# Optimization experiments

Hardware: AMD Instinct MI355X
Metric: run time of the kernel (lower is better)

Reference implementation:

```python
import jax, jax.numpy as jnp
import numpy as np

N_EMBED = 1024
HEAD_SIZE = 64

def setup_inputs() -> dict:
    key = jax.random.key(0)
    kx, kq, kk, kv = jax.random.split(key, 4)
    B, T = 8, 2048
    s = 1.0 / np.sqrt(N_EMBED)
    return {
        "x": jax.random.normal(kx, (B, T, N_EMBED), dtype=jnp.float32),
        "Wq": jax.random.normal(kq, (N_EMBED, HEAD_SIZE), dtype=jnp.float32) * s,
        "Wk": jax.random.normal(kk, (N_EMBED, HEAD_SIZE), dtype=jnp.float32) * s,
        "Wv": jax.random.normal(kv, (N_EMBED, HEAD_SIZE), dtype=jnp.float32) * s,
    }

def reference(x, Wq, Wk, Wv):
    # x: [B,T,C]; W*: [C,H]
    q = x @ Wq  # [B,T,H]
    k = x @ Wk
    v = x @ Wv
    T = x.shape[1]
    scale = jnp.asarray(HEAD_SIZE, x.dtype) ** -0.5
    wei = jnp.einsum("bth,bsh->bts", q, k) * scale  # [B,T,T]
    causal = jnp.tril(jnp.ones((T, T), dtype=bool))
    wei = jnp.where(causal, wei, jnp.asarray(-jnp.inf, wei.dtype))
    wei = jax.nn.softmax(wei, axis=-1)
    # dropout = 0.0 (eval mode): identity
    return jnp.einsum("bts,bsh->bth", wei, v)  # [B,T,H]
```

## Files before the change

kernel.cpp:

```cpp
#include <hip/hip_runtime.h>

#define NB 8
#define NT 2048
#define NC 1024
#define NH 64

typedef __bf16 bf16x8 __attribute__((ext_vector_type(8)));
typedef float f32x4 __attribute__((ext_vector_type(4)));

static __device__ __forceinline__ float4 ldf4(const float* p) {
  return *reinterpret_cast<const float4*>(p);
}
static __device__ __forceinline__ unsigned pack_bf2(float a, float b) {
  unsigned short ua = __builtin_bit_cast(unsigned short, (__bf16)a);
  unsigned short ub = __builtin_bit_cast(unsigned short, (__bf16)b);
  return (unsigned)ua | ((unsigned)ub << 16);
}

__global__ __launch_bounds__(256) void wt_kernel(
    const float* __restrict__ Wq, const float* __restrict__ Wk,
    const float* __restrict__ Wv, __bf16* __restrict__ wt) {
  __shared__ __bf16 tl[64][72];
  const int tid = threadIdx.x;
  const int mat = blockIdx.x >> 4;
  const int k0 = (blockIdx.x & 15) * 64;
  const float* W = (mat == 0) ? Wq : (mat == 1) ? Wk : Wv;
#pragma unroll
  for (int it = 0; it < 4; ++it) {
    int f = tid + it * 256;
    int kk = f >> 4, c4 = (f & 15) * 4;
    float4 w = ldf4(&W[(k0 + kk) * NH + c4]);
    tl[c4 + 0][kk] = (__bf16)w.x;
    tl[c4 + 1][kk] = (__bf16)w.y;
    tl[c4 + 2][kk] = (__bf16)w.z;
    tl[c4 + 3][kk] = (__bf16)w.w;
  }
  __syncthreads();
#pragma unroll
  for (int it = 0; it < 2; ++it) {
    int f = tid + it * 256;
    int h = f >> 3, k8 = (f & 7) * 8;
    *reinterpret_cast<bf16x8*>(&wt[(mat * 64 + h) * NC + k0 + k8]) =
        *reinterpret_cast<const bf16x8*>(&tl[h][k8]);
  }
}

__global__ __launch_bounds__(256, 2) void qkv_mfma_kernel(
    const float* __restrict__ x, const __bf16* __restrict__ wt,
    __bf16* __restrict__ qb, __bf16* __restrict__ kb, __bf16* __restrict__ vt) {
  __shared__ __bf16 As[32][72];
  __shared__ __bf16 Bs[192][72];
  __shared__ __bf16 vls[64][40];
  const int tid = threadIdx.x;
  const int lane = tid & 63;
  const int w = tid >> 6;
  const int row0 = blockIdx.x * 32;
  const int csub = w * 48;
  const int l15 = lane & 15, lg = lane >> 4;

  f32x4 acc[2][3];
#pragma unroll
  for (int i = 0; i < 2; ++i)
#pragma unroll
    for (int j = 0; j < 3; ++j) acc[i][j] = (f32x4){0.f, 0.f, 0.f, 0.f};

  float4 areg[2];
  bf16x8 breg[6];
#pragma unroll
  for (int it = 0; it < 2; ++it) {
    int f = tid + it * 256;
    int r = f >> 4, k4 = (f & 15) * 4;
    areg[it] = ldf4(&x[(row0 + r) * NC + k4]);
  }
#pragma unroll
  for (int it = 0; it < 6; ++it) {
    int f = tid + it * 256;
    int col = f >> 3, k8 = (f & 7) * 8;
    breg[it] = *reinterpret_cast<const bf16x8*>(&wt[col * NC + k8]);
  }

  for (int ch = 0; ch < 16; ++ch) {
#pragma unroll
    for (int it = 0; it < 2; ++it) {
      int f = tid + it * 256;
      int r = f >> 4, k4 = (f & 15) * 4;
      uint2 u = {pack_bf2(areg[it].x, areg[it].y), pack_bf2(areg[it].z, areg[it].w)};
      *reinterpret_cast<uint2*>(&As[r][k4]) = u;
    }
#pragma unroll
    for (int it = 0; it < 6; ++it) {
      int f = tid + it * 256;
      int col = f >> 3, k8 = (f & 7) * 8;
      *reinterpret_cast<bf16x8*>(&Bs[col][k8]) = breg[it];
    }
    __syncthreads();
    if (ch < 15) {
      const int k0n = (ch + 1) * 64;
#pragma unroll
      for (int it = 0; it < 2; ++it) {
        int f = tid + it * 256;
        int r = f >> 4, k4 = (f & 15) * 4;
        areg[it] = ldf4(&x[(row0 + r) * NC + k0n + k4]);
      }
#pragma unroll
      for (int it = 0; it < 6; ++it) {
        int f = tid + it * 256;
        int col = f >> 3, k8 = (f & 7) * 8;
        breg[it] = *reinterpret_cast<const bf16x8*>(&wt[col * NC + k0n + k8]);
      }
    }
#pragma unroll
    for (int kk = 0; kk < 2; ++kk) {
      bf16x8 af[2], bfr[3];
#pragma unroll
      for (int rt = 0; rt < 2; ++rt)
        af[rt] = *reinterpret_cast<const bf16x8*>(&As[rt * 16 + l15][kk * 32 + lg * 8]);
#pragma unroll
      for (int nt = 0; nt < 3; ++nt)
        bfr[nt] = *reinterpret_cast<const bf16x8*>(&Bs[csub + nt * 16 + l15][kk * 32 + lg * 8]);
#pragma unroll
      for (int rt = 0; rt < 2; ++rt)
#pragma unroll
        for (int nt = 0; nt < 3; ++nt)
          acc[rt][nt] = __builtin_amdgcn_mfma_f32_16x16x32_bf16(af[rt], bfr[nt], acc[rt][nt], 0, 0, 0);
    }
    __syncthreads();
  }

#pragma unroll
  for (int rt = 0; rt < 2; ++rt) {
#pragma unroll
    for (int nt = 0; nt < 3; ++nt) {
      int colbase = csub + nt * 16;
      int mat = colbase >> 6;
      int h = (colbase & 63) + l15;
      if (mat == 0) {
#pragma unroll
        for (int r = 0; r < 4; ++r) {
          int row = row0 + rt * 16 + lg * 4 + r;
          qb[row * NH + h] = (__bf16)(acc[rt][nt][r] * 0.125f);
        }
      } else if (mat == 1) {
#pragma unroll
        for (int r = 0; r < 4; ++r) {
          int row = row0 + rt * 16 + lg * 4 + r;
          kb[row * NH + h] = (__bf16)acc[rt][nt][r];
        }
      } else {
        ushort4 pk;
        pk.x = __builtin_bit_cast(unsigned short, (__bf16)acc[rt][nt][0]);
        pk.y = __builtin_bit_cast(unsigned short, (__bf16)acc[rt][nt][1]);
        pk.z = __builtin_bit_cast(unsigned short, (__bf16)acc[rt][nt][2]);
        pk.w = __builtin_bit_cast(unsigned short, (__bf16)acc[rt][nt][3]);
        *reinterpret_cast<ushort4*>(&vls[h][rt * 16 + lg * 4]) = pk;
      }
    }
  }
  __syncthreads();
  {
    int h = tid >> 2, t8 = (tid & 3) * 8;
    int bb = row0 >> 11;
    int t0l = row0 & (NT - 1);
    *reinterpret_cast<bf16x8*>(&vt[((size_t)bb * NH + h) * NT + t0l + t8]) =
        *reinterpret_cast<const bf16x8*>(&vls[h][t8]);
  }
}

__global__ __launch_bounds__(256, 2) void attn_mfma_kernel(
    const __bf16* __restrict__ qb, const __bf16* __restrict__ kb,
    const __bf16* __restrict__ vt, float* __restrict__ out) {
  __shared__ __bf16 ps[4][32][72];
  __shared__ float obuf[4][32][68];
  __shared__ float msh[4][32], lsh[4][32];
  const int tid = threadIdx.x;
  const int lane = tid & 63;
  const int w = tid >> 6;
  const int l15 = lane & 15, lg = lane >> 4;
  const int b = blockIdx.y;
  const int qt = (blockIdx.y < 4) ? (63 - (int)blockIdx.x) : (int)blockIdx.x;
  const int q0 = qt * 32;
  const size_t bT = (size_t)b * NT;

  bf16x8 qf[2][2];
#pragma unroll
  for (int ct = 0; ct < 2; ++ct)
#pragma unroll
    for (int kh = 0; kh < 2; ++kh)
      qf[ct][kh] = *reinterpret_cast<const bf16x8*>(
          &qb[(bT + q0 + ct * 16 + l15) * NH + kh * 32 + lg * 8]);

  float m[2] = {-1e30f, -1e30f};
  float lsum[2] = {0.f, 0.f};
  f32x4 o[2][4];
#pragma unroll
  for (int i = 0; i < 2; ++i)
#pragma unroll
    for (int j = 0; j < 4; ++j) o[i][j] = (f32x4){0.f, 0.f, 0.f, 0.f};

  const int nch = qt / 2 + 1;
  bf16x8 kf[4][2], vf[4][2];
  if (w < nch) {
    const int s0 = w * 64;
#pragma unroll
    for (int st = 0; st < 4; ++st)
#pragma unroll
      for (int kh = 0; kh < 2; ++kh)
        kf[st][kh] = *reinterpret_cast<const bf16x8*>(
            &kb[(bT + s0 + st * 16 + l15) * NH + kh * 32 + lg * 8]);
#pragma unroll
    for (int ht = 0; ht < 4; ++ht)
#pragma unroll
      for (int sh = 0; sh < 2; ++sh)
        vf[ht][sh] = *reinterpret_cast<const bf16x8*>(
            &vt[((size_t)b * NH + ht * 16 + l15) * NT + s0 + sh * 32 + lg * 8]);
  }

  for (int c = w; c < nch; c += 4) {
    const int s0 = c * 64;
    f32x4 s[4][2];
#pragma unroll
    for (int st = 0; st < 4; ++st)
#pragma unroll
      for (int ct = 0; ct < 2; ++ct) s[st][ct] = (f32x4){0.f, 0.f, 0.f, 0.f};
    __builtin_amdgcn_s_setprio(1);
#pragma unroll
    for (int st = 0; st < 4; ++st)
#pragma unroll
      for (int ct = 0; ct < 2; ++ct)
#pragma unroll
        for (int kh = 0; kh < 2; ++kh)
          s[st][ct] = __builtin_amdgcn_mfma_f32_16x16x32_bf16(kf[st][kh], qf[ct][kh], s[st][ct], 0, 0, 0);
    __builtin_amdgcn_s_setprio(0);

    const int cn = c + 4;
    bf16x8 kfn[4][2], vfn[4][2];
    if (cn < nch) {
      const int sn = cn * 64;
#pragma unroll
      for (int st = 0; st < 4; ++st)
#pragma unroll
        for (int kh = 0; kh < 2; ++kh)
          kfn[st][kh] = *reinterpret_cast<const bf16x8*>(
              &kb[(bT + sn + st * 16 + l15) * NH + kh * 32 + lg * 8]);
#pragma unroll
      for (int ht = 0; ht < 4; ++ht)
#pragma unroll
        for (int sh = 0; sh < 2; ++sh)
          vfn[ht][sh] = *reinterpret_cast<const bf16x8*>(
              &vt[((size_t)b * NH + ht * 16 + l15) * NT + sn + sh * 32 + lg * 8]);
    }

    if (s0 + 63 > q0) {
#pragma unroll
      for (int st = 0; st < 4; ++st)
#pragma unroll
        for (int ct = 0; ct < 2; ++ct) {
          int qg = q0 + ct * 16 + l15;
#pragma unroll
          for (int r = 0; r < 4; ++r) {
            int sg = s0 + st * 16 + lg * 4 + r;
            if (sg > qg) s[st][ct][r] = -1e30f;
          }
        }
    }
    float scv[2];
#pragma unroll
    for (int ct = 0; ct < 2; ++ct) {
      float rmx = -1e30f;
#pragma unroll
      for (int st = 0; st < 4; ++st)
#pragma unroll
        for (int r = 0; r < 4; ++r) rmx = fmaxf(rmx, s[st][ct][r]);
      rmx = fmaxf(rmx, __shfl_xor(rmx, 16));
      rmx = fmaxf(rmx, __shfl_xor(rmx, 32));
      float mn = fmaxf(m[ct], rmx);
      float sc = __expf(m[ct] - mn);
      m[ct] = mn;
      float rs = 0.f;
#pragma unroll
      for (int st = 0; st < 4; ++st) {
        float p0 = __expf(s[st][ct][0] - mn);
        float p1 = __expf(s[st][ct][1] - mn);
        float p2 = __expf(s[st][ct][2] - mn);
        float p3 = __expf(s[st][ct][3] - mn);
        rs += (p0 + p1) + (p2 + p3);
        int sp = st * 16 + lg * 4;
        *reinterpret_cast<unsigned*>(&ps[w][ct * 16 + l15][sp]) = pack_bf2(p0, p1);
        *reinterpret_cast<unsigned*>(&ps[w][ct * 16 + l15][sp + 2]) = pack_bf2(p2, p3);
      }
      rs += __shfl_xor(rs, 16);
      rs += __shfl_xor(rs, 32);
      lsum[ct] = lsum[ct] * sc + rs;
      scv[ct] = sc;
    }
#pragma unroll
    for (int rt = 0; rt < 2; ++rt)
#pragma unroll
      for (int r = 0; r < 4; ++r) {
        float fsc = __shfl(scv[rt], lg * 4 + r, 64);
#pragma unroll
        for (int ht = 0; ht < 4; ++ht) o[rt][ht][r] *= fsc;
      }
    __builtin_amdgcn_s_setprio(1);
#pragma unroll
    for (int rt = 0; rt < 2; ++rt) {
      bf16x8 pf[2];
#pragma unroll
      for (int sh = 0; sh < 2; ++sh)
        pf[sh] = *reinterpret_cast<const bf16x8*>(&ps[w][rt * 16 + l15][sh * 32 + lg * 8]);
#pragma unroll
      for (int ht = 0; ht < 4; ++ht)
#pragma unroll
        for (int sh = 0; sh < 2; ++sh)
          o[rt][ht] = __builtin_amdgcn_mfma_f32_16x16x32_bf16(pf[sh], vf[ht][sh], o[rt][ht], 0, 0, 0);
    }
    __builtin_amdgcn_s_setprio(0);
    if (cn < nch) {
#pragma unroll
      for (int st = 0; st < 4; ++st)
#pragma unroll
        for (int kh = 0; kh < 2; ++kh) kf[st][kh] = kfn[st][kh];
#pragma unroll
      for (int ht = 0; ht < 4; ++ht)
#pragma unroll
        for (int sh = 0; sh < 2; ++sh) vf[ht][sh] = vfn[ht][sh];
    }
  }

  if (lg == 0) {
#pragma unroll
    for (int ct = 0; ct < 2; ++ct) {
      msh[w][ct * 16 + l15] = m[ct];
      lsh[w][ct * 16 + l15] = lsum[ct];
    }
  }
#pragma unroll
  for (int rt = 0; rt < 2; ++rt)
#pragma unroll
    for (int ht = 0; ht < 4; ++ht)
#pragma unroll
      for (int r = 0; r < 4; ++r)
        obuf[w][rt * 16 + lg * 4 + r][ht * 16 + l15] = o[rt][ht][r];
  __syncthreads();

  {
    int qr = tid >> 3, h8 = (tid & 7) * 8;
    float m0 = msh[0][qr], m1 = msh[1][qr], m2 = msh[2][qr], m3 = msh[3][qr];
    float M = fmaxf(fmaxf(m0, m1), fmaxf(m2, m3));
    float e0 = __expf(m0 - M), e1 = __expf(m1 - M);
    float e2 = __expf(m2 - M), e3 = __expf(m3 - M);
    float L = e0 * lsh[0][qr] + e1 * lsh[1][qr] + e2 * lsh[2][qr] + e3 * lsh[3][qr];
    float inv = 1.f / L;
#pragma unroll
    for (int i = 0; i < 8; ++i) {
      int h = h8 + i;
      float v = e0 * obuf[0][qr][h] + e1 * obuf[1][qr][h] +
                e2 * obuf[2][qr][h] + e3 * obuf[3][qr][h];
      out[(bT + q0 + qr) * NH + h] = v * inv;
    }
  }
}

extern "C" void kernel_launch(void* const* d_in, const int* in_sizes, int n_in,
                              void* d_out, int out_size, void* d_ws, size_t ws_size,
                              hipStream_t stream) {
  const float* x  = (const float*)d_in[0];
  const float* Wq = (const float*)d_in[1];
  const float* Wk = (const float*)d_in[2];
  const float* Wv = (const float*)d_in[3];
  float* out = (float*)d_out;

  char* ws = (char*)d_ws;
  __bf16* wt = (__bf16*)(ws);
  __bf16* qb = (__bf16*)(ws + 393216);
  __bf16* kb = (__bf16*)(ws + 393216 + 2097152);
  __bf16* vt = (__bf16*)(ws + 393216 + 2 * 2097152);

  wt_kernel<<<dim3(48), dim3(256), 0, stream>>>(Wq, Wk, Wv, wt);
  qkv_mfma_kernel<<<dim3(512), dim3(256), 0, stream>>>(x, wt, qb, kb, vt);
  attn_mfma_kernel<<<dim3(64, 8), dim3(256), 0, stream>>>(qb, kb, vt, out);
}
```

Before: 48.06 us.

## Halve attention query tile to 16 rows, doubling blocks and occupancy

The attention kernel now processes 16 query rows per block instead of 32 and launches 128x8 blocks. Launch bounds rise from 2 to 4 blocks per SM, and the explicit K/V register prefetch for the next chunk is removed, which frees registers. The final output store is vectorised to float4. More blocks should improve load balance and latency hiding on the causal workload. The cost is that each K/V chunk is reloaded by twice as many blocks, and without the prefetch, load latency is exposed inside each iteration.

```diff
diff --git a/kernel.cpp b/kernel.cpp
--- a/kernel.cpp
+++ b/kernel.cpp
@@ -166,198 +166,144 @@
   }
 }
 
-__global__ __launch_bounds__(256, 2) void attn_mfma_kernel(
+__global__ __launch_bounds__(256, 4) void attn_mfma_kernel(
     const __bf16* __restrict__ qb, const __bf16* __restrict__ kb,
     const __bf16* __restrict__ vt, float* __restrict__ out) {
-  __shared__ __bf16 ps[4][32][72];
-  __shared__ float obuf[4][32][68];
-  __shared__ float msh[4][32], lsh[4][32];
+  __shared__ __bf16 ps[4][16][88];
+  __shared__ float obuf[4][16][68];
+  __shared__ float msh[4][16], lsh[4][16];
   const int tid = threadIdx.x;
   const int lane = tid & 63;
   const int w = tid >> 6;
   const int l15 = lane & 15, lg = lane >> 4;
   const int b = blockIdx.y;
-  const int qt = (blockIdx.y < 4) ? (63 - (int)blockIdx.x) : (int)blockIdx.x;
-  const int q0 = qt * 32;
+  const int qt = ((blockIdx.y & 3) < 2) ? (127 - (int)blockIdx.x) : (int)blockIdx.x;
+  const int q0 = qt * 16;
   const size_t bT = (size_t)b * NT;
 
-  bf16x8 qf[2][2];
-#pragma unroll
-  for (int ct = 0; ct < 2; ++ct)
-#pragma unroll
-    for (int kh = 0; kh < 2; ++kh)
-      qf[ct][kh] = *reinterpret_cast<const bf16x8*>(
-          &qb[(bT + q0 + ct * 16 + l15) * NH + kh * 32 + lg * 8]);
-
-  float m[2] = {-1e30f, -1e30f};
-  float lsum[2] = {0.f, 0.f};
-  f32x4 o[2][4];
-#pragma unroll
-  for (int i = 0; i < 2; ++i)
-#pragma unroll
-    for (int j = 0; j < 4; ++j) o[i][j] = (f32x4){0.f, 0.f, 0.f, 0.f};
-
-  const int nch = qt / 2 + 1;
-  bf16x8 kf[4][2], vf[4][2];
-  if (w < nch) {
-    const int s0 = w * 64;
+  bf16x8 qf[2];
+#pragma unroll
+  for (int kh = 0; kh < 2; ++kh)
+    qf[kh] = *reinterpret_cast<const bf16x8*>(
+        &qb[(bT + q0 + l15) * NH + kh * 32 + lg * 8]);
+
+  float m = -1e30f, lsum = 0.f;
+  f32x4 o[4];
+#pragma unroll
+  for (int j = 0; j < 4; ++j) o[j] = (f32x4){0.f, 0.f, 0.f, 0.f};
+
+  const int nch = qt / 4 + 1;
+  for (int c = w; c < nch; c += 4) {
+    const int s0 = c * 64;
+    bf16x8 kf[4][2];
 #pragma unroll
     for (int st = 0; st < 4; ++st)
 #pragma unroll
       for (int kh = 0; kh < 2; ++kh)
         kf[st][kh] = *reinterpret_cast<const bf16x8*>(
             &kb[(bT + s0 + st * 16 + l15) * NH + kh * 32 + lg * 8]);
+    f32x4 s[4];
+#pragma unroll
+    for (int st = 0; st < 4; ++st) s[st] = (f32x4){0.f, 0.f, 0.f, 0.f};
+    __builtin_amdgcn_s_setprio(1);
+#pragma unroll
+    for (int st = 0; st < 4; ++st)
+#pragma unroll
+      for (int kh = 0; kh < 2; ++kh)
+        s[st] = __builtin_amdgcn_mfma_f32_16x16x32_bf16(kf[st][kh], qf[kh], s[st], 0, 0, 0);
+    __builtin_amdgcn_s_setprio(0);
+
+    bf16x8 vf[4][2];
 #pragma unroll
     for (int ht = 0; ht < 4; ++ht)
 #pragma unroll
       for (int sh = 0; sh < 2; ++sh)
         vf[ht][sh] = *reinterpret_cast<const bf16x8*>(
             &vt[((size_t)b * NH + ht * 16 + l15) * NT + s0 + sh * 32 + lg * 8]);
-  }
-
-  for (int c = w; c < nch; c += 4) {
-    const int s0 = c * 64;
-    f32x4 s[4][2];
+
+    if (s0 + 63 > q0) {
+      const int qg = q0 + l15;
+#pragma unroll
+      for (int st = 0; st < 4; ++st)
+#pragma unroll
+        for (int r = 0; r < 4; ++r) {
+          int sg = s0 + st * 16 + lg * 4 + r;
+          if (sg > qg) s[st][r] = -1e30f;
+        }
+    }
+    float rmx = -1e30f;
 #pragma unroll
     for (int st = 0; st < 4; ++st)
 #pragma unroll
-      for (int ct = 0; ct < 2; ++ct) s[st][ct] = (f32x4){0.f, 0.f, 0.f, 0.f};
+      for (int r = 0; r < 4; ++r) rmx = fmaxf(rmx, s[st][r]);
+    rmx = fmaxf(rmx, __shfl_xor(rmx, 16));
+    rmx = fmaxf(rmx, __shfl_xor(rmx, 32));
+    float mn = fmaxf(m, rmx);
+    float sc = __expf(m - mn);
+    m = mn;
+    float rs = 0.f;
+#pragma unroll
+    for (int st = 0; st < 4; ++st) {
+      float p0 = __expf(s[st][0] - mn);
+      float p1 = __expf(s[st][1] - mn);
+      float p2 = __expf(s[st][2] - mn);
+      float p3 = __expf(s[st][3] - mn);
+      rs += (p0 + p1) + (p2 + p3);
+      int sp = st * 16 + lg * 4;
+      *reinterpret_cast<unsigned*>(&ps[w][l15][sp]) = pack_bf2(p0, p1);
+      *reinterpret_cast<unsigned*>(&ps[w][l15][sp + 2]) = pack_bf2(p2, p3);
+    }
+    rs += __shfl_xor(rs, 16);
+    rs += __shfl_xor(rs, 32);
+    lsum = lsum * sc + rs;
+#pragma unroll
+    for (int r = 0; r < 4; ++r) {
+      float fsc = __shfl(sc, lg * 4 + r, 64);
+#pragma unroll
+      for (int ht = 0; ht < 4; ++ht) o[ht][r] *= fsc;
+    }
     __builtin_amdgcn_s_setprio(1);
-#pragma unroll
-    for (int st = 0; st < 4; ++st)
-#pragma unroll
-      for (int ct = 0; ct < 2; ++ct)
-#pragma unroll
-        for (int kh = 0; kh < 2; ++kh)
-          s[st][ct] = __builtin_amdgcn_mfma_f32_16x16x32_bf16(kf[st][kh], qf[ct][kh], s[st][ct], 0, 0, 0);
+    bf16x8 pf[2];
+#pragma unroll
+    for (int sh = 0; sh < 2; ++sh)
+      pf[sh] = *reinterpret_cast<const bf16x8*>(&ps[w][l15][sh * 32 + lg * 8]);
+#pragma unroll
+    for (int ht = 0; ht < 4; ++ht)
+#pragma unroll
+      for (int sh = 0; sh < 2; ++sh)
+        o[ht] = __builtin_amdgcn_mfma_f32_16x16x32_bf16(pf[sh], vf[ht][sh], o[ht], 0, 0, 0);
     __builtin_amdgcn_s_setprio(0);
-
-    const int cn = c + 4;
-    bf16x8 kfn[4][2], vfn[4][2];
-    if (cn < nch) {
-      const int sn = cn * 64;
-#pragma unroll
-      for (int st = 0; st < 4; ++st)
-#pragma unroll
-        for (int kh = 0; kh < 2; ++kh)
-          kfn[st][kh] = *reinterpret_cast<const bf16x8*>(
-              &kb[(bT + sn + st * 16 + l15) * NH + kh * 32 + lg * 8]);
-#pragma unroll
-      for (int ht = 0; ht < 4; ++ht)
-#pragma unroll
-        for (int sh = 0; sh < 2; ++sh)
-          vfn[ht][sh] = *reinterpret_cast<const bf16x8*>(
-              &vt[((size_t)b * NH + ht * 16 + l15) * NT + sn + sh * 32 + lg * 8]);
-    }
-
-    if (s0 + 63 > q0) {
-#pragma unroll
-      for (int st = 0; st < 4; ++st)
-#pragma unroll
-        for (int ct = 0; ct < 2; ++ct) {
-          int qg = q0 + ct * 16 + l15;
-#pragma unroll
-          for (int r = 0; r < 4; ++r) {
-            int sg = s0 + st * 16 + lg * 4 + r;
-            if (sg > qg) s[st][ct][r] = -1e30f;
-          }
-        }
-    }
-    float scv[2];
-#pragma unroll
-    for (int ct = 0; ct < 2; ++ct) {
-      float rmx = -1e30f;
-#pragma unroll
-      for (int st = 0; st < 4; ++st)
-#pragma unroll
-        for (int r = 0; r < 4; ++r) rmx = fmaxf(rmx, s[st][ct][r]);
-      rmx = fmaxf(rmx, __shfl_xor(rmx, 16));
-      rmx = fmaxf(rmx, __shfl_xor(rmx, 32));
-      float mn = fmaxf(m[ct], rmx);
-      float sc = __expf(m[ct] - mn);
-      m[ct] = mn;
-      float rs = 0.f;
-#pragma unroll
-      for (int st = 0; st < 4; ++st) {
-        float p0 = __expf(s[st][ct][0] - mn);
-        float p1 = __expf(s[st][ct][1] - mn);
-        float p2 = __expf(s[st][ct][2] - mn);
-        float p3 = __expf(s[st][ct][3] - mn);
-        rs += (p0 + p1) + (p2 + p3);
-        int sp = st * 16 + lg * 4;
-        *reinterpret_cast<unsigned*>(&ps[w][ct * 16 + l15][sp]) = pack_bf2(p0, p1);
-        *reinterpret_cast<unsigned*>(&ps[w][ct * 16 + l15][sp + 2]) = pack_bf2(p2, p3);
-      }
-      rs += __shfl_xor(rs, 16);
-      rs += __shfl_xor(rs, 32);
-      lsum[ct] = lsum[ct] * sc + rs;
-      scv[ct] = sc;
-    }
-#pragma unroll
-    for (int rt = 0; rt < 2; ++rt)
-#pragma unroll
-      for (int r = 0; r < 4; ++r) {
-        float fsc = __shfl(scv[rt], lg * 4 + r, 64);
-#pragma unroll
-        for (int ht = 0; ht < 4; ++ht) o[rt][ht][r] *= fsc;
-      }
-    __builtin_amdgcn_s_setprio(1);
-#pragma unroll
-    for (int rt = 0; rt < 2; ++rt) {
-      bf16x8 pf[2];
-#pragma unroll
-      for (int sh = 0; sh < 2; ++sh)
-        pf[sh] = *reinterpret_cast<const bf16x8*>(&ps[w][rt * 16 + l15][sh * 32 + lg * 8]);
-#pragma unroll
-      for (int ht = 0; ht < 4; ++ht)
-#pragma unroll
-        for (int sh = 0; sh < 2; ++sh)
-          o[rt][ht] = __builtin_amdgcn_mfma_f32_16x16x32_bf16(pf[sh], vf[ht][sh], o[rt][ht], 0, 0, 0);
-    }
-    __builtin_amdgcn_s_setprio(0);
-    if (cn < nch) {
-#pragma unroll
-      for (int st = 0; st < 4; ++st)
-#pragma unroll
-        for (int kh = 0; kh < 2; ++kh) kf[st][kh] = kfn[st][kh];
-#pragma unroll
-      for (int ht = 0; ht < 4; ++ht)
-#pragma unroll
-        for (int sh = 0; sh < 2; ++sh) vf[ht][sh] = vfn[ht][sh];
-    }
   }
 
   if (lg == 0) {
-#pragma unroll
-    for (int ct = 0; ct < 2; ++ct) {
-      msh[w][ct * 16 + l15] = m[ct];
-      lsh[w][ct * 16 + l15] = lsum[ct];
-    }
-  }
-#pragma unroll
-  for (int rt = 0; rt < 2; ++rt)
-#pragma unroll
-    for (int ht = 0; ht < 4; ++ht)
-#pragma unroll
-      for (int r = 0; r < 4; ++r)
-        obuf[w][rt * 16 + lg * 4 + r][ht * 16 + l15] = o[rt][ht][r];
+    msh[w][l15] = m;
+    lsh[w][l15] = lsum;
+  }
+#pragma unroll
+  for (int ht = 0; ht < 4; ++ht)
+#pragma unroll
+    for (int r = 0; r < 4; ++r)
+      obuf[w][lg * 4 + r][ht * 16 + l15] = o[ht][r];
   __syncthreads();
 
   {
-    int qr = tid >> 3, h8 = (tid & 7) * 8;
+    int qr = tid >> 4, h4 = (tid & 15) * 4;
     float m0 = msh[0][qr], m1 = msh[1][qr], m2 = msh[2][qr], m3 = msh[3][qr];
     float M = fmaxf(fmaxf(m0, m1), fmaxf(m2, m3));
     float e0 = __expf(m0 - M), e1 = __expf(m1 - M);
     float e2 = __expf(m2 - M), e3 = __expf(m3 - M);
     float L = e0 * lsh[0][qr] + e1 * lsh[1][qr] + e2 * lsh[2][qr] + e3 * lsh[3][qr];
     float inv = 1.f / L;
-#pragma unroll
-    for (int i = 0; i < 8; ++i) {
-      int h = h8 + i;
+    float4 res;
+    float* rp = &res.x;
+#pragma unroll
+    for (int i = 0; i < 4; ++i) {
+      int h = h4 + i;
       float v = e0 * obuf[0][qr][h] + e1 * obuf[1][qr][h] +
                 e2 * obuf[2][qr][h] + e3 * obuf[3][qr][h];
-      out[(bT + q0 + qr) * NH + h] = v * inv;
-    }
+      rp[i] = v * inv;
+    }
+    *reinterpret_cast<float4*>(&out[(bT + q0 + qr) * NH + h4]) = res;
   }
 }
 
@@ -378,5 +324,5 @@
 
   wt_kernel<<<dim3(48), dim3(256), 0, stream>>>(Wq, Wk, Wv, wt);
   qkv_mfma_kernel<<<dim3(512), dim3(256), 0, stream>>>(x, wt, qb, kb, vt);
-  attn_mfma_kernel<<<dim3(64, 8), dim3(256), 0, stream>>>(qb, kb, vt, out);
-}
+  attn_mfma_kernel<<<dim3(128, 8), dim3(256), 0, stream>>>(qb, kb, vt, out);
+}
```

Result: slower. 60.40 us (+25.7%).

## Stream QKV weight tiles directly into double-buffered swizzled LDS

Applied to the files above, without the earlier changes.

In the QKV projection kernel, the bf16 weight tile is now copied from global memory straight into LDS with global_load_lds, instead of passing through registers. The weight and activation tiles are double-buffered, and the B tile uses an XOR swizzle in place of row padding to avoid bank conflicts. This lets the trailing per-chunk barrier be dropped and cuts register pressure. It relies on correct ordering between the asynchronous LDS writes and the remaining barrier, and it uses more LDS per block.

```diff
diff --git a/kernel.cpp b/kernel.cpp
--- a/kernel.cpp
+++ b/kernel.cpp
@@ -15,6 +15,11 @@
   unsigned short ua = __builtin_bit_cast(unsigned short, (__bf16)a);
   unsigned short ub = __builtin_bit_cast(unsigned short, (__bf16)b);
   return (unsigned)ua | ((unsigned)ub << 16);
+}
+static __device__ __forceinline__ void gload16(const __bf16* g, __bf16* l) {
+  __builtin_amdgcn_global_load_lds(
+      (const __attribute__((address_space(1))) unsigned int*)g,
+      (__attribute__((address_space(3))) unsigned int*)l, 16, 0, 0);
 }
 
 __global__ __launch_bounds__(256) void wt_kernel(
@@ -48,8 +53,8 @@
 __global__ __launch_bounds__(256, 2) void qkv_mfma_kernel(
     const float* __restrict__ x, const __bf16* __restrict__ wt,
     __bf16* __restrict__ qb, __bf16* __restrict__ kb, __bf16* __restrict__ vt) {
-  __shared__ __bf16 As[32][72];
-  __shared__ __bf16 Bs[192][72];
+  __shared__ __bf16 As[2][32][72];
+  __shared__ __bf16 Bs[2][192][64];
   __shared__ __bf16 vls[64][40];
   const int tid = threadIdx.x;
   const int lane = tid & 63;
@@ -65,7 +70,6 @@
     for (int j = 0; j < 3; ++j) acc[i][j] = (f32x4){0.f, 0.f, 0.f, 0.f};
 
   float4 areg[2];
-  bf16x8 breg[6];
 #pragma unroll
   for (int it = 0; it < 2; ++it) {
     int f = tid + it * 256;
@@ -75,56 +79,54 @@
 #pragma unroll
   for (int it = 0; it < 6; ++it) {
     int f = tid + it * 256;
-    int col = f >> 3, k8 = (f & 7) * 8;
-    breg[it] = *reinterpret_cast<const bf16x8*>(&wt[col * NC + k8]);
+    int col = f >> 3, oct = f & 7;
+    gload16(&wt[col * NC + ((oct ^ (col & 7)) * 8)], &Bs[0][0][0] + f * 8);
   }
 
   for (int ch = 0; ch < 16; ++ch) {
+    const int cur = ch & 1;
 #pragma unroll
     for (int it = 0; it < 2; ++it) {
       int f = tid + it * 256;
       int r = f >> 4, k4 = (f & 15) * 4;
       uint2 u = {pack_bf2(areg[it].x, areg[it].y), pack_bf2(areg[it].z, areg[it].w)};
-      *reinterpret_cast<uint2*>(&As[r][k4]) = u;
-    }
-#pragma unroll
-    for (int it = 0; it < 6; ++it) {
-      int f = tid + it * 256;
-      int col = f >> 3, k8 = (f & 7) * 8;
-      *reinterpret_cast<bf16x8*>(&Bs[col][k8]) = breg[it];
+      *reinterpret_cast<uint2*>(&As[cur][r][k4]) = u;
     }
     __syncthreads();
     if (ch < 15) {
       const int k0n = (ch + 1) * 64;
+      __bf16* bdst = &Bs[1 - cur][0][0];
+#pragma unroll
+      for (int it = 0; it < 6; ++it) {
+        int f = tid + it * 256;
+        int col = f >> 3, oct = f & 7;
+        gload16(&wt[col * NC + k0n + ((oct ^ (col & 7)) * 8)], bdst + f * 8);
+      }
 #pragma unroll
       for (int it = 0; it < 2; ++it) {
         int f = tid + it * 256;
         int r = f >> 4, k4 = (f & 15) * 4;
         areg[it] = ldf4(&x[(row0 + r) * NC + k0n + k4]);
       }
-#pragma unroll
-      for (int it = 0; it < 6; ++it) {
-        int f = tid + it * 256;
-        int col = f >> 3, k8 = (f & 7) * 8;
-        breg[it] = *reinterpret_cast<const bf16x8*>(&wt[col * NC + k0n + k8]);
-      }
     }
 #pragma unroll
     for (int kk = 0; kk < 2; ++kk) {
       bf16x8 af[2], bfr[3];
 #pragma unroll
       for (int rt = 0; rt < 2; ++rt)
-        af[rt] = *reinterpret_cast<const bf16x8*>(&As[rt * 16 + l15][kk * 32 + lg * 8]);
-#pragma unroll
-      for (int nt = 0; nt < 3; ++nt)
-        bfr[nt] = *reinterpret_cast<const bf16x8*>(&Bs[csub + nt * 16 + l15][kk * 32 + lg * 8]);
+        af[rt] = *reinterpret_cast<const bf16x8*>(&As[cur][rt * 16 + l15][kk * 32 + lg * 8]);
+#pragma unroll
+      for (int nt = 0; nt < 3; ++nt) {
+        int col = csub + nt * 16 + l15;
+        int oct = (kk * 4 + lg) ^ (col & 7);
+        bfr[nt] = *reinterpret_cast<const bf16x8*>(&Bs[cur][col][oct * 8]);
+      }
 #pragma unroll
       for (int rt = 0; rt < 2; ++rt)
 #pragma unroll
         for (int nt = 0; nt < 3; ++nt)
           acc[rt][nt] = __builtin_amdgcn_mfma_f32_16x16x32_bf16(af[rt], bfr[nt], acc[rt][nt], 0, 0, 0);
     }
-    __syncthreads();
   }
 
 #pragma unroll
```

After: 52.64 us. 9.5% more time.

## Load QKV projection operands directly from global into registers, dropping LDS staging

Applied to the files above, without the earlier changes.

The QKV projection kernel no longer stages x and weight tiles through shared memory with per-chunk barriers. Each wave now owns a 16-row by 96-column sub-tile, loads its MFMA fragments straight from global memory with a one-step register prefetch, and converts x to bf16 in registers. This removes LDS traffic and the two syncthreads per chunk. In exchange, fragments shared across waves are now reloaded from global or L2 (x twice, weights twice), and the global loads are narrower and strided.

```diff
diff --git a/kernel.cpp b/kernel.cpp
--- a/kernel.cpp
+++ b/kernel.cpp
@@ -11,10 +11,19 @@
 static __device__ __forceinline__ float4 ldf4(const float* p) {
   return *reinterpret_cast<const float4*>(p);
 }
+static __device__ __forceinline__ bf16x8 ldb8(const __bf16* p) {
+  return *reinterpret_cast<const bf16x8*>(p);
+}
 static __device__ __forceinline__ unsigned pack_bf2(float a, float b) {
   unsigned short ua = __builtin_bit_cast(unsigned short, (__bf16)a);
   unsigned short ub = __builtin_bit_cast(unsigned short, (__bf16)b);
   return (unsigned)ua | ((unsigned)ub << 16);
+}
+static __device__ __forceinline__ bf16x8 cvt8(float4 a, float4 b) {
+  bf16x8 r;
+  r[0] = (__bf16)a.x; r[1] = (__bf16)a.y; r[2] = (__bf16)a.z; r[3] = (__bf16)a.w;
+  r[4] = (__bf16)b.x; r[5] = (__bf16)b.y; r[6] = (__bf16)b.z; r[7] = (__bf16)b.w;
+  return r;
 }
 
 __global__ __launch_bounds__(256) void wt_kernel(
@@ -48,112 +57,74 @@
 __global__ __launch_bounds__(256, 2) void qkv_mfma_kernel(
     const float* __restrict__ x, const __bf16* __restrict__ wt,
     __bf16* __restrict__ qb, __bf16* __restrict__ kb, __bf16* __restrict__ vt) {
-  __shared__ __bf16 As[32][72];
-  __shared__ __bf16 Bs[192][72];
   __shared__ __bf16 vls[64][40];
   const int tid = threadIdx.x;
   const int lane = tid & 63;
   const int w = tid >> 6;
+  const int wr = w >> 1, wc = w & 1;
   const int row0 = blockIdx.x * 32;
-  const int csub = w * 48;
   const int l15 = lane & 15, lg = lane >> 4;
 
-  f32x4 acc[2][3];
-#pragma unroll
-  for (int i = 0; i < 2; ++i)
-#pragma unroll
-    for (int j = 0; j < 3; ++j) acc[i][j] = (f32x4){0.f, 0.f, 0.f, 0.f};
-
-  float4 areg[2];
-  bf16x8 breg[6];
-#pragma unroll
-  for (int it = 0; it < 2; ++it) {
-    int f = tid + it * 256;
-    int r = f >> 4, k4 = (f & 15) * 4;
-    areg[it] = ldf4(&x[(row0 + r) * NC + k4]);
-  }
-#pragma unroll
-  for (int it = 0; it < 6; ++it) {
-    int f = tid + it * 256;
-    int col = f >> 3, k8 = (f & 7) * 8;
-    breg[it] = *reinterpret_cast<const bf16x8*>(&wt[col * NC + k8]);
-  }
-
-  for (int ch = 0; ch < 16; ++ch) {
-#pragma unroll
-    for (int it = 0; it < 2; ++it) {
-      int f = tid + it * 256;
-      int r = f >> 4, k4 = (f & 15) * 4;
-      uint2 u = {pack_bf2(areg[it].x, areg[it].y), pack_bf2(areg[it].z, areg[it].w)};
-      *reinterpret_cast<uint2*>(&As[r][k4]) = u;
-    }
-#pragma unroll
-    for (int it = 0; it < 6; ++it) {
-      int f = tid + it * 256;
-      int col = f >> 3, k8 = (f & 7) * 8;
-      *reinterpret_cast<bf16x8*>(&Bs[col][k8]) = breg[it];
-    }
-    __syncthreads();
-    if (ch < 15) {
-      const int k0n = (ch + 1) * 64;
-#pragma unroll
-      for (int it = 0; it < 2; ++it) {
-        int f = tid + it * 256;
-        int r = f >> 4, k4 = (f & 15) * 4;
-        areg[it] = ldf4(&x[(row0 + r) * NC + k0n + k4]);
+  f32x4 acc[6];
+#pragma unroll
+  for (int j = 0; j < 6; ++j) acc[j] = (f32x4){0.f, 0.f, 0.f, 0.f};
+
+  const float* xr = &x[(size_t)(row0 + wr * 16 + l15) * NC + lg * 8];
+  const __bf16* wb = &wt[(size_t)(wc * 96 + l15) * NC + lg * 8];
+
+  float4 a0 = ldf4(xr), a1 = ldf4(xr + 4);
+  bf16x8 b[6];
+#pragma unroll
+  for (int nt = 0; nt < 6; ++nt) b[nt] = ldb8(wb + nt * 16 * NC);
+
+#pragma unroll
+  for (int ks = 0; ks < 32; ++ks) {
+    float4 a0n, a1n;
+    bf16x8 bn[6];
+    if (ks < 31) {
+      const int off = (ks + 1) * 32;
+      a0n = ldf4(xr + off);
+      a1n = ldf4(xr + off + 4);
+#pragma unroll
+      for (int nt = 0; nt < 6; ++nt) bn[nt] = ldb8(wb + nt * 16 * NC + off);
+    }
+    bf16x8 af = cvt8(a0, a1);
+#pragma unroll
+    for (int nt = 0; nt < 6; ++nt)
+      acc[nt] = __builtin_amdgcn_mfma_f32_16x16x32_bf16(af, b[nt], acc[nt], 0, 0, 0);
+    if (ks < 31) {
+      a0 = a0n; a1 = a1n;
+#pragma unroll
+      for (int nt = 0; nt < 6; ++nt) b[nt] = bn[nt];
+    }
+  }
+
+#pragma unroll
+  for (int nt = 0; nt < 6; ++nt) {
+    const int colbase = wc * 96 + nt * 16;
+    const int mat = colbase >> 6;
+    if (mat == 0) {
+      const int h = (colbase & 63) + l15;
+#pragma unroll
+      for (int r = 0; r < 4; ++r) {
+        int row = row0 + wr * 16 + lg * 4 + r;
+        qb[row * NH + h] = (__bf16)(acc[nt][r] * 0.125f);
       }
-#pragma unroll
-      for (int it = 0; it < 6; ++it) {
-        int f = tid + it * 256;
-        int col = f >> 3, k8 = (f & 7) * 8;
-        breg[it] = *reinterpret_cast<const bf16x8*>(&wt[col * NC + k0n + k8]);
+    } else if (mat == 1) {
+      const int h = (colbase & 63) + l15;
+#pragma unroll
+      for (int r = 0; r < 4; ++r) {
+        int row = row0 + wr * 16 + lg * 4 + r;
+        kb[row * NH + h] = (__bf16)acc[nt][r];
       }
-    }
-#pragma unroll
-    for (int kk = 0; kk < 2; ++kk) {
-      bf16x8 af[2], bfr[3];
-#pragma unroll
-      for (int rt = 0; rt < 2; ++rt)
-        af[rt] = *reinterpret_cast<const bf16x8*>(&As[rt * 16 + l15][kk * 32 + lg * 8]);
-#pragma unroll
-      for (int nt = 0; nt < 3; ++nt)
-        bfr[nt] = *reinterpret_cast<const bf16x8*>(&Bs[csub + nt * 16 + l15][kk * 32 + lg * 8]);
-#pragma unroll
-      for (int rt = 0; rt < 2; ++rt)
-#pragma unroll
-        for (int nt = 0; nt < 3; ++nt)
-          acc[rt][nt] = __builtin_amdgcn_mfma_f32_16x16x32_bf16(af[rt], bfr[nt], acc[rt][nt], 0, 0, 0);
-    }
-    __syncthreads();
-  }
-
-#pragma unroll
-  for (int rt = 0; rt < 2; ++rt) {
-#pragma unroll
-    for (int nt = 0; nt < 3; ++nt) {
-      int colbase = csub + nt * 16;
-      int mat = colbase >> 6;
-      int h = (colbase & 63) + l15;
-      if (mat == 0) {
-#pragma unroll
-        for (int r = 0; r < 4; ++r) {
-          int row = row0 + rt * 16 + lg * 4 + r;
-          qb[row * NH + h] = (__bf16)(acc[rt][nt][r] * 0.125f);
-        }
-      } else if (mat == 1) {
-#pragma unroll
-        for (int r = 0; r < 4; ++r) {
-          int row = row0 + rt * 16 + lg * 4 + r;
-          kb[row * NH + h] = (__bf16)acc[rt][nt][r];
-        }
-      } else {
-        ushort4 pk;
-        pk.x = __builtin_bit_cast(unsigned short, (__bf16)acc[rt][nt][0]);
-        pk.y = __builtin_bit_cast(unsigned short, (__bf16)acc[rt][nt][1]);
-        pk.z = __builtin_bit_cast(unsigned short, (__bf16)acc[rt][nt][2]);
-        pk.w = __builtin_bit_cast(unsigned short, (__bf16)acc[rt][nt][3]);
-        *reinterpret_cast<ushort4*>(&vls[h][rt * 16 + lg * 4]) = pk;
-      }
+    } else {
+      const int h = (colbase - 128) + l15;
+      ushort4 pk;
+      pk.x = __builtin_bit_cast(unsigned short, (__bf16)acc[nt][0]);
+      pk.y = __builtin_bit_cast(unsigned short, (__bf16)acc[nt][1]);
+      pk.z = __builtin_bit_cast(unsigned short, (__bf16)acc[nt][2]);
+      pk.w = __builtin_bit_cast(unsigned short, (__bf16)acc[nt][3]);
+      *reinterpret_cast<ushort4*>(&vls[h][wr * 16 + lg * 4]) = pk;
     }
   }
   __syncthreads();
```

Measured after the change: 87.82 us. +82.7%, slower.
